# Performance work log

Measured on AMD Instinct MI355X. Metric: run time of the kernel, lower is better.

## Reference

```python
import jax, jax.numpy as jnp
import numpy as np

EMBED_DIM = 1024
NUM_HEADS = 16
HEAD_DIM = EMBED_DIM // NUM_HEADS
SEG_LEN = 1024  # all segment_lengths equal, dilation_rate == 1


def setup_inputs() -> dict:
    key = jax.random.key(0)
    k1, k2, k3 = jax.random.split(key, 3)
    B, S, E = 2, 4096, EMBED_DIM
    x = jax.random.normal(k1, (B, S, E), dtype=jnp.float32)
    w_qkv = jax.random.normal(k2, (3 * E, E), dtype=jnp.float32) * (E ** -0.5)
    b_qkv = jnp.zeros((3 * E,), dtype=jnp.float32)
    w_out = jax.random.normal(k3, (E, E), dtype=jnp.float32) * (E ** -0.5)
    b_out = jnp.zeros((E,), dtype=jnp.float32)
    return {"x": x, "w_qkv": w_qkv, "b_qkv": b_qkv, "w_out": w_out, "b_out": b_out}


def reference(x, w_qkv, b_qkv, w_out, b_out):
    B, S, E = x.shape
    H, Dh = NUM_HEADS, HEAD_DIM
    scale = 1.0 / np.sqrt(Dh).astype(np.float32)
    # QKV projection
    qkv = x @ w_qkv.T + b_qkv                      # [B, S, 3E]
    qkv = qkv.reshape(B, S, 3, H, Dh).transpose(2, 0, 3, 1, 4)  # [3, B, H, S, Dh]
    q, k, v = qkv[0], qkv[1], qkv[2]
    # Segments tile the sequence; each query attends only within its segment
    # (block-diagonal attention; online-softmax combine across segments is
    # trivial since the segments are disjoint in the query dimension).
    n = S // SEG_LEN
    q = q.reshape(B, H, n, SEG_LEN, Dh)
    k = k.reshape(B, H, n, SEG_LEN, Dh)
    v = v.reshape(B, H, n, SEG_LEN, Dh)
    scores = jnp.einsum("bhnqd,bhnkd->bhnqk", q, k) * scale
    attn = jax.nn.softmax(scores, axis=-1)
    out = jnp.einsum("bhnqk,bhnkd->bhnqd", attn, v)  # [B, H, n, seg, Dh]
    out = out.reshape(B, H, S, Dh).transpose(0, 2, 1, 3).reshape(B, S, E)
    return out @ w_out.T + b_out
```

## Files before the change

### kernel.cpp

```cpp
#include <hip/hip_runtime.h>

typedef __bf16 bf16x8 __attribute__((ext_vector_type(8)));
typedef float f32x4 __attribute__((ext_vector_type(4)));

#define SL2E 0.18033688011112042f

__device__ __forceinline__ unsigned short f2bf(float f) {
  union { float f; unsigned u; } v; v.f = f;
  unsigned r = v.u + 0x7fffu + ((v.u >> 16) & 1u);
  return (unsigned short)(r >> 16);
}

__device__ __forceinline__ float fast_exp2(float x) {
#if __has_builtin(__builtin_amdgcn_exp2f)
  return __builtin_amdgcn_exp2f(x);
#else
  return exp2f(x);
#endif
}

__device__ __forceinline__ unsigned pack_bf2(float lo, float hi) {
  union { float f; unsigned u; } a, b;
  a.f = lo; b.f = hi;
#if __has_builtin(__builtin_amdgcn_perm)
  return __builtin_amdgcn_perm(b.u + 0x7fffu, a.u + 0x7fffu, 0x07060302u);
#else
  return ((b.u + 0x7fffu) & 0xffff0000u) | ((a.u + 0x7fffu) >> 16);
#endif
}

__device__ __forceinline__ void gload16(const unsigned short* g, unsigned short* l) {
  __builtin_amdgcn_global_load_lds(
      (const __attribute__((address_space(1))) unsigned int*)g,
      (__attribute__((address_space(3))) unsigned int*)l, 16, 0, 0);
}

#define SWZ(r, cg) ((((r) * 8) + ((cg) ^ ((r) & 7))) * 8)

__global__ __launch_bounds__(256) void f32_to_bf16_all(
    const float* __restrict__ x, const float* __restrict__ wq, const float* __restrict__ wo,
    unsigned short* __restrict__ xb, unsigned short* __restrict__ wqb, unsigned short* __restrict__ wob) {
  int i = blockIdx.x * 256 + threadIdx.x;
  const float* src; unsigned short* dst; int off;
  if (i < 2097152) { src = x; dst = xb; off = i; }
  else if (i < 2883584) { src = wq; dst = wqb; off = i - 2097152; }
  else if (i < 3145728) { src = wo; dst = wob; off = i - 2883584; }
  else return;
  float4 v = ((const float4*)src)[off];
  ushort4 o;
  o.x = f2bf(v.x); o.y = f2bf(v.y); o.z = f2bf(v.z); o.w = f2bf(v.w);
  ((ushort4*)dst)[off] = o;
}


template <bool SWAP>
__device__ __forceinline__ void qkv_tile_compute(
    const unsigned short* Acur, const unsigned short* Bcur,
    int l15, int quad, int wm, int wn, f32x4 acc[4][4]) {
#pragma unroll
  for (int kk = 0; kk < 2; ++kk) {
    int swk = (((kk * 4 + quad) ^ (l15 & 7))) * 8;
    bf16x8 af[4], bfr[4];
#pragma unroll
    for (int i = 0; i < 4; ++i) af[i] = *(const bf16x8*)(Acur + (wm + i * 16 + l15) * 64 + swk);
#pragma unroll
    for (int j = 0; j < 4; ++j) bfr[j] = *(const bf16x8*)(Bcur + (wn + j * 16 + l15) * 64 + swk);
    if constexpr (SWAP) {
#pragma unroll
      for (int j = 0; j < 4; ++j)
#pragma unroll
        for (int i = 0; i < 4; ++i)
          acc[j][i] = __builtin_amdgcn_mfma_f32_16x16x32_bf16(bfr[j], af[i], acc[j][i], 0, 0, 0);
    } else {
#pragma unroll
      for (int i = 0; i < 4; ++i)
#pragma unroll
        for (int j = 0; j < 4; ++j)
          acc[i][j] = __builtin_amdgcn_mfma_f32_16x16x32_bf16(af[i], bfr[j], acc[i][j], 0, 0, 0);
    }
  }
}

template <bool SWAP>
__device__ __forceinline__ void gemm_mainloop_dbuf(
    const unsigned short* Ag, const unsigned short* Bg,
    unsigned short* A0, unsigned short* B0,
    unsigned short* A1, unsigned short* B1,
    int w, int l15, int quad, int wm, int wn, f32x4 acc[4][4]) {
  const int K = 1024;
  unsigned short* Aw[2] = {A0 + w * 2048, A1 + w * 2048};
  unsigned short* Bw[2] = {B0 + w * 2048, B1 + w * 2048};
#pragma unroll
  for (int i = 0; i < 4; ++i) {
    gload16(Ag + i * 8 * K, Aw[0] + i * 512);
    gload16(Bg + i * 8 * K, Bw[0] + i * 512);
  }
#pragma unroll 1
  for (int kt2 = 0; kt2 < 16; kt2 += 2) {
#pragma unroll
    for (int i = 0; i < 4; ++i) {
      gload16(Ag + i * 8 * K + (kt2 + 1) * 64, Aw[1] + i * 512);
      gload16(Bg + i * 8 * K + (kt2 + 1) * 64, Bw[1] + i * 512);
    }
    asm volatile("s_waitcnt vmcnt(8)" ::: "memory");
    __builtin_amdgcn_s_barrier();
    __builtin_amdgcn_sched_barrier(0);
    qkv_tile_compute<SWAP>(A0, B0, l15, quad, wm, wn, acc);
    __builtin_amdgcn_s_barrier();
    if (kt2 < 14) {
#pragma unroll
      for (int i = 0; i < 4; ++i) {
        gload16(Ag + i * 8 * K + (kt2 + 2) * 64, Aw[0] + i * 512);
        gload16(Bg + i * 8 * K + (kt2 + 2) * 64, Bw[0] + i * 512);
      }
      asm volatile("s_waitcnt vmcnt(8)" ::: "memory");
    } else {
      asm volatile("s_waitcnt vmcnt(0)" ::: "memory");
    }
    __builtin_amdgcn_s_barrier();
    __builtin_amdgcn_sched_barrier(0);
    qkv_tile_compute<SWAP>(A1, B1, l15, quad, wm, wn, acc);
    __builtin_amdgcn_s_barrier();
  }
}

__global__ __launch_bounds__(256) void gemm_qkv(
    const unsigned short* __restrict__ A,
    const unsigned short* __restrict__ Bt,
    const float* __restrict__ bias,
    unsigned short* __restrict__ Qb,
    unsigned short* __restrict__ Kb,
    unsigned short* __restrict__ Vtb) {
  const int K = 1024;
  __shared__ unsigned short As[2][8192];
  __shared__ unsigned short Bs[2][8192];
  int tid = threadIdx.x;
  int m0 = blockIdx.x * 128, n0 = blockIdx.y * 128;
  int w = tid >> 6, lane = tid & 63, l15 = lane & 15, quad = lane >> 4;
  int wm = (w & 1) * 64, wn = (w >> 1) * 64;

  f32x4 acc[4][4] = {};

  int rs = w * 32 + (lane >> 3);
  int cs = ((lane & 7) ^ (lane >> 3)) * 8;
  const unsigned short* Ag = A + (m0 + rs) * K + cs;
  const unsigned short* Bg = Bt + (n0 + rs) * K + cs;

  int t = n0 >> 10;
  int b = m0 >> 12;

  if (t != 2) {
    gemm_mainloop_dbuf<true>(Ag, Bg, &As[0][0], &Bs[0][0], &As[1][0], &Bs[1][0],
                             w, l15, quad, wm, wn, acc);
    unsigned short* dst = (t == 0) ? Qb : Kb;
    float sc = (t == 0) ? SL2E : 1.0f;
    int h = ((n0 + wn) >> 6) & 15;
    int head_base = (b * 16 + h) * 4096 * 64;
    int s_base = (m0 & 4095) + wm;
#pragma unroll
    for (int j = 0; j < 4; ++j) {
      int d0 = j * 16 + quad * 4;
      float4 bv = *(const float4*)(bias + n0 + wn + d0);
#pragma unroll
      for (int i = 0; i < 4; ++i) {
        int s = s_base + i * 16 + l15;
        ushort4 pk;
        pk.x = f2bf((acc[j][i][0] + bv.x) * sc);
        pk.y = f2bf((acc[j][i][1] + bv.y) * sc);
        pk.z = f2bf((acc[j][i][2] + bv.z) * sc);
        pk.w = f2bf((acc[j][i][3] + bv.w) * sc);
        *(ushort4*)(dst + head_base + s * 64 + d0) = pk;
      }
    }
  } else {
    gemm_mainloop_dbuf<false>(Ag, Bg, &As[0][0], &Bs[0][0], &As[1][0], &Bs[1][0],
                              w, l15, quad, wm, wn, acc);
    int sblk = (m0 & 4095) + wm + quad * 4;
#pragma unroll
    for (int j = 0; j < 4; ++j) {
      int n_j = n0 + wn + j * 16 + l15;
      float bv = bias[n_j];
      int h = (n_j >> 6) & 15, d = n_j & 63;
      int vbase = ((b * 16 + h) * 64 + d) * 4096;
#pragma unroll
      for (int i = 0; i < 4; ++i) {
        int s = sblk + i * 16;
        ushort4 pk;
        pk.x = f2bf(acc[i][j][0] + bv);
        pk.y = f2bf(acc[i][j][1] + bv);
        pk.z = f2bf(acc[i][j][2] + bv);
        pk.w = f2bf(acc[i][j][3] + bv);
        *(ushort4*)(Vtb + vbase + s) = pk;
      }
    }
  }
}

#define LDP 72

__global__ __launch_bounds__(256) void attn_k(
    const unsigned short* __restrict__ Qb,
    const unsigned short* __restrict__ Kb,
    const unsigned short* __restrict__ Vtb,
    unsigned short* __restrict__ Ab) {
  __shared__ unsigned short KV[2][2][4096];
  __shared__ unsigned short Ps[4][16 * LDP];

  int tid = threadIdx.x;
  int idx = blockIdx.x;
  int grp = ((idx >> 5) << 3) | (idx & 7);
  int qblk = (idx >> 3) & 3;
  int seg = grp & 3, h = (grp >> 2) & 15, b = grp >> 6;
  int w = tid >> 6, lane = tid & 63, l15 = lane & 15, quad = lane >> 4;
  int bh = b * 16 + h;
  int q0 = seg * 1024 + qblk * 256 + w * 64;

  const unsigned short* Kg = Kb + (bh * 4096 + seg * 1024) * 64;
  const unsigned short* Vg = Vtb + bh * 64 * 4096 + seg * 1024;

  int r0 = w * 16 + (lane >> 3);
  int cs = ((lane & 7) ^ (lane >> 3)) * 8;

  const unsigned short* Qg = Qb + (bh * 4096 + q0) * 64;
  bf16x8 qf[4][2];
#pragma unroll
  for (int qb = 0; qb < 4; ++qb)
#pragma unroll
    for (int kk = 0; kk < 2; ++kk)
      qf[qb][kk] = *(const bf16x8*)(Qg + (qb * 16 + l15) * 64 + kk * 32 + quad * 8);

  f32x4 o[4][4] = {};
  float lsum[4] = {0.f, 0.f, 0.f, 0.f};
  unsigned short* Pw = Ps[w];

  {
    unsigned short* dk = &KV[0][0][w * 1024];
    unsigned short* dv = &KV[0][1][w * 1024];
    gload16(Kg + r0 * 64 + cs, dk);
    gload16(Kg + (r0 + 8) * 64 + cs, dk + 512);
    gload16(Vg + r0 * 4096 + cs, dv);
    gload16(Vg + (r0 + 8) * 4096 + cs, dv + 512);
  }

#pragma unroll 2
  for (int kt = 0; kt < 16; ++kt) {
    int cur = kt & 1;
    __syncthreads();
    if (kt < 15) {
      unsigned short* dk = &KV[cur ^ 1][0][w * 1024];
      unsigned short* dv = &KV[cur ^ 1][1][w * 1024];
      const unsigned short* kN = Kg + (kt + 1) * 4096;
      const unsigned short* vN = Vg + (kt + 1) * 64;
      gload16(kN + r0 * 64 + cs, dk);
      gload16(kN + (r0 + 8) * 64 + cs, dk + 512);
      gload16(vN + r0 * 4096 + cs, dv);
      gload16(vN + (r0 + 8) * 4096 + cs, dv + 512);
    }
    const unsigned short* Kt = KV[cur][0];
    const unsigned short* Vt = KV[cur][1];

    uint2 pp[4][4];
#pragma unroll
    for (int half = 0; half < 2; ++half) {
      f32x4 st[2][4] = {};
#pragma unroll
      for (int kk = 0; kk < 2; ++kk) {
        int cg = kk * 4 + quad;
        bf16x8 kf0 = *(const bf16x8*)(Kt + SWZ(half * 32 + l15, cg));
        bf16x8 kf1 = *(const bf16x8*)(Kt + SWZ(half * 32 + 16 + l15, cg));
#pragma unroll
        for (int qb = 0; qb < 4; ++qb) {
          st[0][qb] = __builtin_amdgcn_mfma_f32_16x16x32_bf16(kf0, qf[qb][kk], st[0][qb], 0, 0, 0);
          st[1][qb] = __builtin_amdgcn_mfma_f32_16x16x32_bf16(kf1, qf[qb][kk], st[1][qb], 0, 0, 0);
        }
      }
#pragma unroll
      for (int kb = 0; kb < 2; ++kb)
#pragma unroll
        for (int qb = 0; qb < 4; ++qb) {
          f32x4 s = st[kb][qb];
          float p0 = fast_exp2(s[0]), p1 = fast_exp2(s[1]);
          float p2 = fast_exp2(s[2]), p3 = fast_exp2(s[3]);
          lsum[qb] += (p0 + p1) + (p2 + p3);
          uint2 d;
          d.x = pack_bf2(p0, p1);
          d.y = pack_bf2(p2, p3);
          pp[qb][half * 2 + kb] = d;
        }
    }

    bf16x8 vf[2][4];
#pragma unroll
    for (int kk = 0; kk < 2; ++kk)
#pragma unroll
      for (int db = 0; db < 4; ++db)
        vf[kk][db] = *(const bf16x8*)(Vt + SWZ(db * 16 + l15, kk * 4 + quad));
#pragma unroll
    for (int qb = 0; qb < 4; ++qb) {
#pragma unroll
      for (int g = 0; g < 4; ++g)
        *(uint2*)(Pw + l15 * LDP + g * 16 + quad * 4) = pp[qb][g];
#pragma unroll
      for (int kk = 0; kk < 2; ++kk) {
        bf16x8 pa = *(const bf16x8*)(Pw + l15 * LDP + kk * 32 + quad * 8);
#pragma unroll
        for (int db = 0; db < 4; ++db)
          o[qb][db] = __builtin_amdgcn_mfma_f32_16x16x32_bf16(pa, vf[kk][db], o[qb][db], 0, 0, 0);
      }
    }
  }

#pragma unroll
  for (int qb = 0; qb < 4; ++qb) {
    lsum[qb] += __shfl_xor(lsum[qb], 16);
    lsum[qb] += __shfl_xor(lsum[qb], 32);
  }

  float* Wf = (float*)(&KV[0][0][0]) + w * 1024;
#pragma unroll
  for (int qb = 0; qb < 4; ++qb) {
#pragma unroll
    for (int db = 0; db < 4; ++db)
#pragma unroll
      for (int r = 0; r < 4; ++r)
        Wf[(quad * 4 + r) * 64 + db * 16 + l15] = o[qb][db][r];
    float inv = 1.0f / lsum[qb];
    float4 x0 = *(float4*)(Wf + l15 * 64 + quad * 8);
    float4 x1 = *(float4*)(Wf + l15 * 64 + quad * 8 + 4);
    float4 x2 = *(float4*)(Wf + l15 * 64 + (quad + 4) * 8);
    float4 x3 = *(float4*)(Wf + l15 * 64 + (quad + 4) * 8 + 4);
    uint4 u0, u1;
    u0.x = pack_bf2(x0.x * inv, x0.y * inv);
    u0.y = pack_bf2(x0.z * inv, x0.w * inv);
    u0.z = pack_bf2(x1.x * inv, x1.y * inv);
    u0.w = pack_bf2(x1.z * inv, x1.w * inv);
    u1.x = pack_bf2(x2.x * inv, x2.y * inv);
    u1.y = pack_bf2(x2.z * inv, x2.w * inv);
    u1.z = pack_bf2(x3.x * inv, x3.y * inv);
    u1.w = pack_bf2(x3.z * inv, x3.w * inv);
    int sg = q0 + qb * 16 + l15;
    int base = (b * 4096 + sg) * 1024 + h * 64;
    *(uint4*)(Ab + base + quad * 8) = u0;
    *(uint4*)(Ab + base + (quad + 4) * 8) = u1;
  }
}

__global__ __launch_bounds__(256) void gemm_out(
    const unsigned short* __restrict__ A,
    const unsigned short* __restrict__ Bt,
    const float* __restrict__ bias,
    float* __restrict__ C) {
  const int K = 1024;
  __shared__ unsigned short As2[128 * 64];
  __shared__ unsigned short Bs2[128 * 64];
  int tid = threadIdx.x;
  int m0 = blockIdx.x * 128, n0 = blockIdx.y * 128;
  int w = tid >> 6, lane = tid & 63, l15 = lane & 15, quad = lane >> 4;
  int wm = (w & 1) * 64, wn = (w >> 1) * 64;

  f32x4 acc[4][4] = {};

  int rs = w * 32 + (lane >> 3);
  int cs = ((lane & 7) ^ (lane >> 3)) * 8;
  const unsigned short* Ag = A + (m0 + rs) * K + cs;
  const unsigned short* Bg = Bt + (n0 + rs) * K + cs;
  unsigned short* Asl = As2 + w * 2048;
  unsigned short* Bsl = Bs2 + w * 2048;

  for (int kt = 0; kt < K; kt += 64) {
    __syncthreads();
#pragma unroll
    for (int i = 0; i < 4; ++i) {
      gload16(Ag + i * 8 * K + kt, Asl + i * 512);
      gload16(Bg + i * 8 * K + kt, Bsl + i * 512);
    }
    __syncthreads();
#pragma unroll
    for (int kk = 0; kk < 2; ++kk) {
      int swk = (((kk * 4 + quad) ^ (l15 & 7))) * 8;
      bf16x8 af[4], bfr[4];
#pragma unroll
      for (int i = 0; i < 4; ++i) af[i] = *(const bf16x8*)(As2 + (wm + i * 16 + l15) * 64 + swk);
#pragma unroll
      for (int j = 0; j < 4; ++j) bfr[j] = *(const bf16x8*)(Bs2 + (wn + j * 16 + l15) * 64 + swk);
#pragma unroll
      for (int j = 0; j < 4; ++j)
#pragma unroll
        for (int i = 0; i < 4; ++i)
          acc[j][i] = __builtin_amdgcn_mfma_f32_16x16x32_bf16(bfr[j], af[i], acc[j][i], 0, 0, 0);
    }
  }

#pragma unroll
  for (int j = 0; j < 4; ++j) {
    int nb = n0 + wn + j * 16 + quad * 4;
    float4 bv = *(const float4*)(bias + nb);
#pragma unroll
    for (int i = 0; i < 4; ++i) {
      int m = m0 + wm + i * 16 + l15;
      float4 ov;
      ov.x = acc[j][i][0] + bv.x;
      ov.y = acc[j][i][1] + bv.y;
      ov.z = acc[j][i][2] + bv.z;
      ov.w = acc[j][i][3] + bv.w;
      *(float4*)(C + m * 1024 + nb) = ov;
    }
  }
}

extern "C" void kernel_launch(void* const* d_in, const int* in_sizes, int n_in,
                              void* d_out, int out_size, void* d_ws, size_t ws_size,
                              hipStream_t stream) {
  const float* x     = (const float*)d_in[0];
  const float* w_qkv = (const float*)d_in[1];
  const float* b_qkv = (const float*)d_in[2];
  const float* w_out = (const float*)d_in[3];
  const float* b_out = (const float*)d_in[4];
  float* out = (float*)d_out;
  char* ws = (char*)d_ws;

  unsigned short* wqkvb = (unsigned short*)(ws);
  unsigned short* woutb = (unsigned short*)(ws + 6291456);
  unsigned short* Qb    = (unsigned short*)(ws + 8388608);
  unsigned short* Kb    = (unsigned short*)(ws + 25165824);
  unsigned short* Vtb   = (unsigned short*)(ws + 41943040);
  unsigned short* xb    = (unsigned short*)(ws + 58720256);
  unsigned short* Ab    = xb;

  f32_to_bf16_all<<<12288, 256, 0, stream>>>(x, w_qkv, w_out, xb, wqkvb, woutb);
  gemm_qkv<<<dim3(64, 24), 256, 0, stream>>>(xb, wqkvb, b_qkv, Qb, Kb, Vtb);
  attn_k<<<512, 256, 0, stream>>>(Qb, Kb, Vtb, Ab);
  gemm_out<<<dim3(64, 8), 256, 0, stream>>>(Ab, woutb, b_out, out);
}
```

Baseline: 239.5 us.

## Enlarge QKV GEMM tile to 256x192 and double-buffer output GEMM

```diff
diff --git a/kernel.cpp b/kernel.cpp
--- a/kernel.cpp
+++ b/kernel.cpp
@@ -54,77 +54,64 @@
 
 
 template <bool SWAP>
-__device__ __forceinline__ void qkv_tile_compute(
-    const unsigned short* Acur, const unsigned short* Bcur,
-    int l15, int quad, int wm, int wn, f32x4 acc[4][4]) {
+__device__ __forceinline__ void tile_compute_6x4(
+    const unsigned short* As_, const unsigned short* Bs_,
+    int l15, int quad, int wm, int wn, f32x4* acc) {
 #pragma unroll
   for (int kk = 0; kk < 2; ++kk) {
-    int swk = (((kk * 4 + quad) ^ (l15 & 7))) * 8;
-    bf16x8 af[4], bfr[4];
-#pragma unroll
-    for (int i = 0; i < 4; ++i) af[i] = *(const bf16x8*)(Acur + (wm + i * 16 + l15) * 64 + swk);
-#pragma unroll
-    for (int j = 0; j < 4; ++j) bfr[j] = *(const bf16x8*)(Bcur + (wn + j * 16 + l15) * 64 + swk);
+    int cg = kk * 4 + quad;
+    bf16x8 af[4], bfr[6];
+#pragma unroll
+    for (int i = 0; i < 4; ++i) af[i] = *(const bf16x8*)(As_ + SWZ(wm + i * 16 + l15, cg));
+#pragma unroll
+    for (int j = 0; j < 6; ++j) bfr[j] = *(const bf16x8*)(Bs_ + SWZ(wn + j * 16 + l15, cg));
     if constexpr (SWAP) {
 #pragma unroll
-      for (int j = 0; j < 4; ++j)
+      for (int j = 0; j < 6; ++j)
 #pragma unroll
         for (int i = 0; i < 4; ++i)
-          acc[j][i] = __builtin_amdgcn_mfma_f32_16x16x32_bf16(bfr[j], af[i], acc[j][i], 0, 0, 0);
+          acc[j * 4 + i] = __builtin_amdgcn_mfma_f32_16x16x32_bf16(bfr[j], af[i], acc[j * 4 + i], 0, 0, 0);
     } else {
 #pragma unroll
       for (int i = 0; i < 4; ++i)
 #pragma unroll
-        for (int j = 0; j < 4; ++j)
-          acc[i][j] = __builtin_amdgcn_mfma_f32_16x16x32_bf16(af[i], bfr[j], acc[i][j], 0, 0, 0);
+        for (int j = 0; j < 6; ++j)
+          acc[i * 6 + j] = __builtin_amdgcn_mfma_f32_16x16x32_bf16(af[i], bfr[j], acc[i * 6 + j], 0, 0, 0);
     }
   }
 }
 
 template <bool SWAP>
-__device__ __forceinline__ void gemm_mainloop_dbuf(
-    const unsigned short* Ag, const unsigned short* Bg,
-    unsigned short* A0, unsigned short* B0,
-    unsigned short* A1, unsigned short* B1,
-    int w, int l15, int quad, int wm, int wn, f32x4 acc[4][4]) {
-  const int K = 1024;
-  unsigned short* Aw[2] = {A0 + w * 2048, A1 + w * 2048};
-  unsigned short* Bw[2] = {B0 + w * 2048, B1 + w * 2048};
-#pragma unroll
-  for (int i = 0; i < 4; ++i) {
-    gload16(Ag + i * 8 * K, Aw[0] + i * 512);
-    gload16(Bg + i * 8 * K, Bw[0] + i * 512);
-  }
+__device__ __forceinline__ void mainloop_256x192(
+    const unsigned short* const srcp[7], const int ldso[7],
+    unsigned short* lds0, unsigned short* lds1,
+    int l15, int quad, int wm, int wn, f32x4* acc) {
+#pragma unroll
+  for (int i = 0; i < 7; ++i) gload16(srcp[i], lds0 + ldso[i]);
 #pragma unroll 1
-  for (int kt2 = 0; kt2 < 16; kt2 += 2) {
-#pragma unroll
-    for (int i = 0; i < 4; ++i) {
-      gload16(Ag + i * 8 * K + (kt2 + 1) * 64, Aw[1] + i * 512);
-      gload16(Bg + i * 8 * K + (kt2 + 1) * 64, Bw[1] + i * 512);
-    }
-    asm volatile("s_waitcnt vmcnt(8)" ::: "memory");
+  for (int t2 = 0; t2 < 16; t2 += 2) {
+#pragma unroll
+    for (int i = 0; i < 7; ++i) gload16(srcp[i] + (t2 + 1) * 64, lds1 + ldso[i]);
+    asm volatile("s_waitcnt vmcnt(7)" ::: "memory");
     __builtin_amdgcn_s_barrier();
     __builtin_amdgcn_sched_barrier(0);
-    qkv_tile_compute<SWAP>(A0, B0, l15, quad, wm, wn, acc);
+    tile_compute_6x4<SWAP>(lds0, lds0 + 16384, l15, quad, wm, wn, acc);
     __builtin_amdgcn_s_barrier();
-    if (kt2 < 14) {
-#pragma unroll
-      for (int i = 0; i < 4; ++i) {
-        gload16(Ag + i * 8 * K + (kt2 + 2) * 64, Aw[0] + i * 512);
-        gload16(Bg + i * 8 * K + (kt2 + 2) * 64, Bw[0] + i * 512);
-      }
-      asm volatile("s_waitcnt vmcnt(8)" ::: "memory");
+    if (t2 < 14) {
+#pragma unroll
+      for (int i = 0; i < 7; ++i) gload16(srcp[i] + (t2 + 2) * 64, lds0 + ldso[i]);
+      asm volatile("s_waitcnt vmcnt(7)" ::: "memory");
     } else {
       asm volatile("s_waitcnt vmcnt(0)" ::: "memory");
     }
     __builtin_amdgcn_s_barrier();
     __builtin_amdgcn_sched_barrier(0);
-    qkv_tile_compute<SWAP>(A1, B1, l15, quad, wm, wn, acc);
+    tile_compute_6x4<SWAP>(lds1, lds1 + 16384, l15, quad, wm, wn, acc);
     __builtin_amdgcn_s_barrier();
   }
 }
 
-__global__ __launch_bounds__(256) void gemm_qkv(
+__global__ __launch_bounds__(512, 2) void gemm_qkv(
     const unsigned short* __restrict__ A,
     const unsigned short* __restrict__ Bt,
     const float* __restrict__ bias,
@@ -132,52 +119,59 @@
     unsigned short* __restrict__ Kb,
     unsigned short* __restrict__ Vtb) {
   const int K = 1024;
-  __shared__ unsigned short As[2][8192];
-  __shared__ unsigned short Bs[2][8192];
+  __shared__ unsigned short SMEM[2][28672];
   int tid = threadIdx.x;
-  int m0 = blockIdx.x * 128, n0 = blockIdx.y * 128;
   int w = tid >> 6, lane = tid & 63, l15 = lane & 15, quad = lane >> 4;
-  int wm = (w & 1) * 64, wn = (w >> 1) * 64;
-
-  f32x4 acc[4][4] = {};
-
-  int rs = w * 32 + (lane >> 3);
-  int cs = ((lane & 7) ^ (lane >> 3)) * 8;
-  const unsigned short* Ag = A + (m0 + rs) * K + cs;
-  const unsigned short* Bg = Bt + (n0 + rs) * K + cs;
-
-  int t = n0 >> 10;
+  int m0 = blockIdx.x * 256, n0 = blockIdx.y * 192;
+  int wm = (w & 3) * 64, wn = (w >> 2) * 96;
   int b = m0 >> 12;
 
-  if (t != 2) {
-    gemm_mainloop_dbuf<true>(Ag, Bg, &As[0][0], &Bs[0][0], &As[1][0], &Bs[1][0],
-                             w, l15, quad, wm, wn, acc);
-    unsigned short* dst = (t == 0) ? Qb : Kb;
-    float sc = (t == 0) ? SL2E : 1.0f;
-    int h = ((n0 + wn) >> 6) & 15;
-    int head_base = (b * 16 + h) * 4096 * 64;
+  int rlane = lane >> 3;
+  int cs = ((lane & 7) ^ rlane) * 8;
+  const unsigned short* srcp[7];
+  int ldso[7];
+#pragma unroll
+  for (int i = 0; i < 7; ++i) {
+    int q = w * 7 + i;
+    if (q < 32) { srcp[i] = A + (m0 + q * 8 + rlane) * K + cs; ldso[i] = q * 512; }
+    else { srcp[i] = Bt + (n0 + (q - 32) * 8 + rlane) * K + cs; ldso[i] = 16384 + (q - 32) * 512; }
+  }
+
+  f32x4 acc[24] = {};
+
+  bool pureV = (n0 >= 2048);
+  bool mixed = (n0 < 2048) && (n0 + 192 > 2048);
+
+  if (!pureV && !mixed) {
+    mainloop_256x192<true>(srcp, ldso, &SMEM[0][0], &SMEM[1][0], l15, quad, wm, wn, acc);
     int s_base = (m0 & 4095) + wm;
 #pragma unroll
-    for (int j = 0; j < 4; ++j) {
-      int d0 = j * 16 + quad * 4;
-      float4 bv = *(const float4*)(bias + n0 + wn + d0);
+    for (int j = 0; j < 6; ++j) {
+      int ng = n0 + wn + j * 16;
+      int t = ng >> 10;
+      unsigned short* dst = t ? Kb : Qb;
+      float sc = t ? 1.0f : SL2E;
+      int h = (ng >> 6) & 15;
+      int d0 = (ng & 63) + quad * 4;
+      float4 bv = *(const float4*)(bias + ng + quad * 4);
+      int head_base = (b * 16 + h) * 4096 * 64;
 #pragma unroll
       for (int i = 0; i < 4; ++i) {
         int s = s_base + i * 16 + l15;
+        f32x4 a = acc[j * 4 + i];
         ushort4 pk;
-        pk.x = f2bf((acc[j][i][0] + bv.x) * sc);
-        pk.y = f2bf((acc[j][i][1] + bv.y) * sc);
-        pk.z = f2bf((acc[j][i][2] + bv.z) * sc);
-        pk.w = f2bf((acc[j][i][3] + bv.w) * sc);
+        pk.x = f2bf((a[0] + bv.x) * sc);
+        pk.y = f2bf((a[1] + bv.y) * sc);
+        pk.z = f2bf((a[2] + bv.z) * sc);
+        pk.w = f2bf((a[3] + bv.w) * sc);
         *(ushort4*)(dst + head_base + s * 64 + d0) = pk;
       }
     }
-  } else {
-    gemm_mainloop_dbuf<false>(Ag, Bg, &As[0][0], &Bs[0][0], &As[1][0], &Bs[1][0],
-                              w, l15, quad, wm, wn, acc);
+  } else if (pureV) {
+    mainloop_256x192<false>(srcp, ldso, &SMEM[0][0], &SMEM[1][0], l15, quad, wm, wn, acc);
     int sblk = (m0 & 4095) + wm + quad * 4;
 #pragma unroll
-    for (int j = 0; j < 4; ++j) {
+    for (int j = 0; j < 6; ++j) {
       int n_j = n0 + wn + j * 16 + l15;
       float bv = bias[n_j];
       int h = (n_j >> 6) & 15, d = n_j & 63;
@@ -185,12 +179,51 @@
 #pragma unroll
       for (int i = 0; i < 4; ++i) {
         int s = sblk + i * 16;
+        f32x4 a = acc[i * 6 + j];
         ushort4 pk;
-        pk.x = f2bf(acc[i][j][0] + bv);
-        pk.y = f2bf(acc[i][j][1] + bv);
-        pk.z = f2bf(acc[i][j][2] + bv);
-        pk.w = f2bf(acc[i][j][3] + bv);
+        pk.x = f2bf(a[0] + bv);
+        pk.y = f2bf(a[1] + bv);
+        pk.z = f2bf(a[2] + bv);
+        pk.w = f2bf(a[3] + bv);
         *(ushort4*)(Vtb + vbase + s) = pk;
+      }
+    }
+  } else {
+    mainloop_256x192<false>(srcp, ldso, &SMEM[0][0], &SMEM[1][0], l15, quad, wm, wn, acc);
+#pragma unroll
+    for (int j = 0; j < 6; ++j) {
+      int ng = n0 + wn + j * 16;
+      if (ng >= 2048) {
+        int n_j = ng + l15;
+        float bv = bias[n_j];
+        int h = (n_j >> 6) & 15, d = n_j & 63;
+        int vbase = ((b * 16 + h) * 64 + d) * 4096;
+        int sblk = (m0 & 4095) + wm + quad * 4;
+#pragma unroll
+        for (int i = 0; i < 4; ++i) {
+          int s = sblk + i * 16;
+          f32x4 a = acc[i * 6 + j];
+          ushort4 pk;
+          pk.x = f2bf(a[0] + bv);
+          pk.y = f2bf(a[1] + bv);
+          pk.z = f2bf(a[2] + bv);
+          pk.w = f2bf(a[3] + bv);
+          *(ushort4*)(Vtb + vbase + s) = pk;
+        }
+      } else {
+        int n_j = ng + l15;
+        float bv = bias[n_j];
+        int h = (n_j >> 6) & 15, d = n_j & 63;
+        int kbase = (b * 16 + h) * 4096 * 64 + d;
+#pragma unroll
+        for (int i = 0; i < 4; ++i) {
+          f32x4 a = acc[i * 6 + j];
+#pragma unroll
+          for (int r = 0; r < 4; ++r) {
+            int s = (m0 & 4095) + wm + i * 16 + quad * 4 + r;
+            Kb[kbase + s * 64] = f2bf(a[r] + bv);
+          }
+        }
       }
     }
   }
@@ -351,8 +384,8 @@
     const float* __restrict__ bias,
     float* __restrict__ C) {
   const int K = 1024;
-  __shared__ unsigned short As2[128 * 64];
-  __shared__ unsigned short Bs2[128 * 64];
+  __shared__ unsigned short As2[2][8192];
+  __shared__ unsigned short Bs2[2][8192];
   int tid = threadIdx.x;
   int m0 = blockIdx.x * 128, n0 = blockIdx.y * 128;
   int w = tid >> 6, lane = tid & 63, l15 = lane & 15, quad = lane >> 4;
@@ -364,30 +397,48 @@
   int cs = ((lane & 7) ^ (lane >> 3)) * 8;
   const unsigned short* Ag = A + (m0 + rs) * K + cs;
   const unsigned short* Bg = Bt + (n0 + rs) * K + cs;
-  unsigned short* Asl = As2 + w * 2048;
-  unsigned short* Bsl = Bs2 + w * 2048;
-
-  for (int kt = 0; kt < K; kt += 64) {
-    __syncthreads();
-#pragma unroll
-    for (int i = 0; i < 4; ++i) {
-      gload16(Ag + i * 8 * K + kt, Asl + i * 512);
-      gload16(Bg + i * 8 * K + kt, Bsl + i * 512);
-    }
-    __syncthreads();
-#pragma unroll
-    for (int kk = 0; kk < 2; ++kk) {
-      int swk = (((kk * 4 + quad) ^ (l15 & 7))) * 8;
-      bf16x8 af[4], bfr[4];
-#pragma unroll
-      for (int i = 0; i < 4; ++i) af[i] = *(const bf16x8*)(As2 + (wm + i * 16 + l15) * 64 + swk);
-#pragma unroll
-      for (int j = 0; j < 4; ++j) bfr[j] = *(const bf16x8*)(Bs2 + (wn + j * 16 + l15) * 64 + swk);
-#pragma unroll
-      for (int j = 0; j < 4; ++j)
-#pragma unroll
-        for (int i = 0; i < 4; ++i)
-          acc[j][i] = __builtin_amdgcn_mfma_f32_16x16x32_bf16(bfr[j], af[i], acc[j][i], 0, 0, 0);
+
+#pragma unroll
+  for (int i = 0; i < 4; ++i) {
+    gload16(Ag + i * 8 * K, &As2[0][0] + w * 2048 + i * 512);
+    gload16(Bg + i * 8 * K, &Bs2[0][0] + w * 2048 + i * 512);
+  }
+#pragma unroll 1
+  for (int kt2 = 0; kt2 < 16; kt2 += 2) {
+#pragma unroll
+    for (int half = 0; half < 2; ++half) {
+      int kt = kt2 + half;
+      unsigned short* Awr = half ? &As2[0][0] : &As2[1][0];
+      unsigned short* Bwr = half ? &Bs2[0][0] : &Bs2[1][0];
+      const unsigned short* Ard = half ? &As2[1][0] : &As2[0][0];
+      const unsigned short* Brd = half ? &Bs2[1][0] : &Bs2[0][0];
+      if (kt < 15) {
+#pragma unroll
+        for (int i = 0; i < 4; ++i) {
+          gload16(Ag + i * 8 * K + (kt + 1) * 64, Awr + w * 2048 + i * 512);
+          gload16(Bg + i * 8 * K + (kt + 1) * 64, Bwr + w * 2048 + i * 512);
+        }
+        asm volatile("s_waitcnt vmcnt(8)" ::: "memory");
+      } else {
+        asm volatile("s_waitcnt vmcnt(0)" ::: "memory");
+      }
+      __builtin_amdgcn_s_barrier();
+      __builtin_amdgcn_sched_barrier(0);
+#pragma unroll
+      for (int kk = 0; kk < 2; ++kk) {
+        int swk = (((kk * 4 + quad) ^ (l15 & 7))) * 8;
+        bf16x8 af[4], bfr[4];
+#pragma unroll
+        for (int i = 0; i < 4; ++i) af[i] = *(const bf16x8*)(Ard + (wm + i * 16 + l15) * 64 + swk);
+#pragma unroll
+        for (int j = 0; j < 4; ++j) bfr[j] = *(const bf16x8*)(Brd + (wn + j * 16 + l15) * 64 + swk);
+#pragma unroll
+        for (int j = 0; j < 4; ++j)
+#pragma unroll
+          for (int i = 0; i < 4; ++i)
+            acc[j][i] = __builtin_amdgcn_mfma_f32_16x16x32_bf16(bfr[j], af[i], acc[j][i], 0, 0, 0);
+      }
+      __builtin_amdgcn_s_barrier();
     }
   }
 
@@ -428,7 +479,7 @@
   unsigned short* Ab    = xb;
 
   f32_to_bf16_all<<<12288, 256, 0, stream>>>(x, w_qkv, w_out, xb, wqkvb, woutb);
-  gemm_qkv<<<dim3(64, 24), 256, 0, stream>>>(xb, wqkvb, b_qkv, Qb, Kb, Vtb);
+  gemm_qkv<<<dim3(32, 16), 512, 0, stream>>>(xb, wqkvb, b_qkv, Qb, Kb, Vtb);
   attn_k<<<512, 256, 0, stream>>>(Qb, Kb, Vtb, Ab);
   gemm_out<<<dim3(64, 8), 256, 0, stream>>>(Ab, woutb, b_out, out);
 }
```

Result: faster. 231.3 us (-3.4%).
